# Optimization experiments

Hardware: AMD Instinct MI355X
Metric: run time of the kernel (lower is better)

Reference implementation:

```python
import jax, jax.numpy as jnp
import numpy as np

B = 8
D_MODEL = 512
N_HEADS = 8
D_HEAD = 64
D_FF = 2048
N_ENC = 4
N_DEC = 4
SRC_LEN = 512
TGT_LEN = 512
PRED_LEN = 96
SRC_SIZE = 16
TGT_SIZE = 8
EPS = 1e-5
W_SCALE = 0.02


def setup_inputs() -> dict:
    key = jax.random.key(0)
    ks = iter(jax.random.split(key, 64))

    def w(shape):
        return jax.random.normal(next(ks), shape, dtype=jnp.float32) * W_SCALE

    d, f = D_MODEL, D_FF
    inp = {
        "src": jax.random.normal(next(ks), (B, SRC_LEN, SRC_SIZE), dtype=jnp.float32),
        "tgt": jax.random.normal(next(ks), (B, TGT_LEN, TGT_SIZE), dtype=jnp.float32),
        "src_pos_emb": w((SRC_LEN, d)),
        "tgt_pos_emb": w((TGT_LEN, d)),
        "src_lin_w": w((SRC_SIZE, d)), "src_lin_b": jnp.zeros((d,), jnp.float32),
        "tgt_lin_w": w((TGT_SIZE, d)), "tgt_lin_b": jnp.zeros((d,), jnp.float32),
        # encoder stacks [N_ENC, ...]
        "enc_wq": w((N_ENC, d, d)), "enc_wk": w((N_ENC, d, d)),
        "enc_wv": w((N_ENC, d, d)), "enc_wo": w((N_ENC, d, d)),
        "enc_ff1_w": w((N_ENC, d, f)), "enc_ff1_b": jnp.zeros((N_ENC, f), jnp.float32),
        "enc_ff2_w": w((N_ENC, f, d)), "enc_ff2_b": jnp.zeros((N_ENC, d), jnp.float32),
        "enc_ln1_g": jnp.ones((N_ENC, d), jnp.float32), "enc_ln1_b": jnp.zeros((N_ENC, d), jnp.float32),
        "enc_ln2_g": jnp.ones((N_ENC, d), jnp.float32), "enc_ln2_b": jnp.zeros((N_ENC, d), jnp.float32),
        # decoder stacks [N_DEC, ...]
        "dec_sa_wq": w((N_DEC, d, d)), "dec_sa_wk": w((N_DEC, d, d)),
        "dec_sa_wv": w((N_DEC, d, d)), "dec_sa_wo": w((N_DEC, d, d)),
        "dec_ca_wq": w((N_DEC, d, d)), "dec_ca_wk": w((N_DEC, d, d)),
        "dec_ca_wv": w((N_DEC, d, d)), "dec_ca_wo": w((N_DEC, d, d)),
        "dec_ff1_w": w((N_DEC, d, f)), "dec_ff1_b": jnp.zeros((N_DEC, f), jnp.float32),
        "dec_ff2_w": w((N_DEC, f, d)), "dec_ff2_b": jnp.zeros((N_DEC, d), jnp.float32),
        "dec_ln1_g": jnp.ones((N_DEC, d), jnp.float32), "dec_ln1_b": jnp.zeros((N_DEC, d), jnp.float32),
        "dec_ln2_g": jnp.ones((N_DEC, d), jnp.float32), "dec_ln2_b": jnp.zeros((N_DEC, d), jnp.float32),
        "dec_ln3_g": jnp.ones((N_DEC, d), jnp.float32), "dec_ln3_b": jnp.zeros((N_DEC, d), jnp.float32),
        "proj_w": w((d, TGT_SIZE)), "proj_b": jnp.zeros((TGT_SIZE,), jnp.float32),
    }
    return inp


def layer_norm(x, g, b):
    mu = jnp.mean(x, axis=-1, keepdims=True)
    var = jnp.mean(jnp.square(x - mu), axis=-1, keepdims=True)
    return (x - mu) * jax.lax.rsqrt(var + EPS) * g + b


def mha(x_q, x_kv, wq, wk, wv, wo, mask):
    Bq, Lq, _ = x_q.shape
    Lk = x_kv.shape[1]
    q = (x_q @ wq).reshape(Bq, Lq, N_HEADS, D_HEAD)
    k = (x_kv @ wk).reshape(Bq, Lk, N_HEADS, D_HEAD)
    v = (x_kv @ wv).reshape(Bq, Lk, N_HEADS, D_HEAD)
    scores = jnp.einsum("bqhd,bkhd->bhqk", q, k) / jnp.sqrt(
        jnp.asarray(D_HEAD, jnp.float32))
    if mask is not None:
        scores = scores + mask  # broadcast over batch/heads
    attn = jax.nn.softmax(scores, axis=-1)
    ctx = jnp.einsum("bhqk,bkhd->bqhd", attn, v).reshape(Bq, Lq, N_HEADS * D_HEAD)
    return ctx @ wo


def dec_self_mask():
    # get_subsequence_mask with pt=0: -inf on last PRED_LEN key columns
    m = jnp.zeros((TGT_LEN, TGT_LEN), jnp.float32)
    return m.at[:, -PRED_LEN:].set(-jnp.inf)


def reference(src, tgt, src_pos_emb, tgt_pos_emb, src_lin_w, src_lin_b,
              tgt_lin_w, tgt_lin_b,
              enc_wq, enc_wk, enc_wv, enc_wo, enc_ff1_w, enc_ff1_b,
              enc_ff2_w, enc_ff2_b, enc_ln1_g, enc_ln1_b, enc_ln2_g, enc_ln2_b,
              dec_sa_wq, dec_sa_wk, dec_sa_wv, dec_sa_wo,
              dec_ca_wq, dec_ca_wk, dec_ca_wv, dec_ca_wo,
              dec_ff1_w, dec_ff1_b, dec_ff2_w, dec_ff2_b,
              dec_ln1_g, dec_ln1_b, dec_ln2_g, dec_ln2_b, dec_ln3_g, dec_ln3_b,
              proj_w, proj_b):
    # input projections + positional embedding (dropout disabled, eval mode)
    enc_x = src_pos_emb[None] + src @ src_lin_w + src_lin_b
    dec_x = tgt_pos_emb[None] + tgt @ tgt_lin_w + tgt_lin_b

    # encoder (enc_self_attn_mask is None)
    for i in range(N_ENC):
        a = mha(enc_x, enc_x, enc_wq[i], enc_wk[i], enc_wv[i], enc_wo[i], None)
        enc_x = layer_norm(a + enc_x, enc_ln1_g[i], enc_ln1_b[i])
        h = jax.nn.relu(enc_x @ enc_ff1_w[i] + enc_ff1_b[i]) @ enc_ff2_w[i] + enc_ff2_b[i]
        enc_x = layer_norm(h + enc_x, enc_ln2_g[i], enc_ln2_b[i])

    sa_mask = dec_self_mask()  # [tgt_len, tgt_len]
    for i in range(N_DEC):
        a = mha(dec_x, dec_x, dec_sa_wq[i], dec_sa_wk[i], dec_sa_wv[i],
                dec_sa_wo[i], sa_mask)
        dec_x = layer_norm(a + dec_x, dec_ln1_g[i], dec_ln1_b[i])
        a = mha(dec_x, enc_x, dec_ca_wq[i], dec_ca_wk[i], dec_ca_wv[i],
                dec_ca_wo[i], None)
        dec_x = layer_norm(a + dec_x, dec_ln2_g[i], dec_ln2_b[i])
        h = jax.nn.relu(dec_x @ dec_ff1_w[i] + dec_ff1_b[i]) @ dec_ff2_w[i] + dec_ff2_b[i]
        dec_x = layer_norm(h + dec_x, dec_ln3_g[i], dec_ln3_b[i])

    return dec_x @ proj_w + proj_b  # [B, tgt_len, tgt_size]
```

## Files before the change

### kernel.cpp

```cpp
#include <hip/hip_runtime.h>
#include <hip/hip_bf16.h>
#include <math.h>

#define D_MODEL 512
#define N_HEADS 8
#define D_HEAD  64
#define D_FF    2048
#define SEQ     512
#define BATCH   8
#define ROWS    (BATCH * SEQ)
#define PRED_LEN 96
#define KLEN_MASKED (SEQ - PRED_LEN)
#define LN_EPS  1e-5f

typedef float  f32x4 __attribute__((ext_vector_type(4)));
typedef short  s16x8 __attribute__((ext_vector_type(8)));

__device__ __forceinline__ float bf2f(ushort u) {
    union { unsigned int i; float f; } c; c.i = ((unsigned int)u) << 16; return c.f;
}
__device__ __forceinline__ ushort f2bf(float v) {
    __hip_bfloat16 h = __float2bfloat16(v);
    return *(ushort*)&h;
}
__device__ __forceinline__ void gl_lds16(const void* g, void* lds) {
    __builtin_amdgcn_global_load_lds(
        (const __attribute__((address_space(1))) unsigned int*)g,
        (__attribute__((address_space(3))) unsigned int*)lds, 16, 0, 0);
}

struct GDesc {
    const ushort* A; int lda;
    const ushort* Bt; int ldb;
    ushort* C; int ldc;
    int N; int K;
    const float* bias; int relu;
    ushort* VT; int vcol0;
};

template<int BN>
__device__ __forceinline__ void gemm_body(const GDesc& d)
{
    constexpr int NW = BN / 32;
    __shared__ __attribute__((aligned(16))) ushort As[2][128 * 32];
    __shared__ __attribute__((aligned(16))) ushort Bs[2][BN * 32];
    const int tid = threadIdx.x;
    const int w = tid >> 6, lane = tid & 63;
    const int l16 = lane & 15, quad = lane >> 4;
    const int m0 = blockIdx.y * 128, n0 = blockIdx.x * BN;
    const ushort* Ab = d.A + (size_t)m0 * d.lda;
    const ushort* Bb = d.Bt + (size_t)n0 * d.ldb;
    const int wm = (w >> 1) * 64, wn = (w & 1) * (BN / 2);
    const int nk = d.K >> 5;

    auto stage = [&](int buf, int k0) {
        #pragma unroll
        for (int q = 0; q < 2; ++q) {
            int c = (q * 4 + w) * 64 + lane;
            int row = c >> 2, ch = (c & 3) ^ ((row >> 1) & 3);
            gl_lds16(Ab + (size_t)row * d.lda + k0 + ch * 8,
                     (void*)(As[buf] + (size_t)(q * 4 + w) * 512));
        }
        #pragma unroll
        for (int q = 0; q < BN / 64; ++q) {
            int c = (q * 4 + w) * 64 + lane;
            int row = c >> 2, ch = (c & 3) ^ ((row >> 1) & 3);
            gl_lds16(Bb + (size_t)row * d.ldb + k0 + ch * 8,
                     (void*)(Bs[buf] + (size_t)(q * 4 + w) * 512));
        }
    };

    f32x4 acc[4][NW];
    #pragma unroll
    for (int i = 0; i < 4; ++i)
        #pragma unroll
        for (int j = 0; j < NW; ++j) acc[i][j] = (f32x4)0.f;

    auto compute = [&](int buf) {
        s16x8 af[4];
        #pragma unroll
        for (int i = 0; i < 4; ++i) {
            int r = wm + i * 16 + l16;
            af[i] = *(const s16x8*)(As[buf] + (size_t)r * 32 + (quad ^ ((r >> 1) & 3)) * 8);
        }
        #pragma unroll
        for (int j = 0; j < NW; ++j) {
            int r = wn + j * 16 + l16;
            s16x8 bfr = *(const s16x8*)(Bs[buf] + (size_t)r * 32 + (quad ^ ((r >> 1) & 3)) * 8);
            #pragma unroll
            for (int i = 0; i < 4; ++i)
                acc[i][j] = __builtin_amdgcn_mfma_f32_16x16x32_bf16(af[i], bfr, acc[i][j], 0, 0, 0);
        }
    };

    stage(0, 0);
    __syncthreads();
    int cur = 0;
    for (int t = 0; t < nk - 1; ++t) {
        stage(cur ^ 1, (t + 1) << 5);
        compute(cur);
        __syncthreads();
        cur ^= 1;
    }
    compute(cur);

    const bool isv = (d.VT != nullptr) && (n0 >= d.vcol0);
    if (isv) {
        #pragma unroll
        for (int i = 0; i < 4; ++i) {
            int mrow = m0 + wm + i * 16 + quad * 4;
            int b = mrow >> 9, pbase = mrow & 511;
            #pragma unroll
            for (int j = 0; j < NW; ++j) {
                int cv = n0 + wn + j * 16 + l16 - d.vcol0;
                int h = cv >> 6, dd = cv & 63;
                union { ushort u[4]; uint2 v; } pk;
                #pragma unroll
                for (int r = 0; r < 4; ++r) pk.u[r] = f2bf(acc[i][j][r]);
                *(uint2*)(d.VT + ((size_t)((b * 8 + h) * 64 + dd) * 512 + pbase)) = pk.v;
            }
        }
    } else {
        #pragma unroll
        for (int i = 0; i < 4; ++i) {
            #pragma unroll
            for (int j = 0; j < NW; ++j) {
                int col = n0 + wn + j * 16 + l16;
                float bv = d.bias ? d.bias[col] : 0.f;
                #pragma unroll
                for (int r = 0; r < 4; ++r) {
                    float v = acc[i][j][r] + bv;
                    if (d.relu) v = fmaxf(v, 0.f);
                    d.C[(size_t)(m0 + wm + i * 16 + quad * 4 + r) * d.ldc + col] = f2bf(v);
                }
            }
        }
    }
}

template<int BN>
__global__ __launch_bounds__(256) void gemm_one(GDesc d)
{
    if ((int)(blockIdx.x * BN) < d.N) gemm_body<BN>(d);
}

__global__ __launch_bounds__(256) void gemm_two(GDesc d0, GDesc d1)
{
    const GDesc& d = blockIdx.z ? d1 : d0;
    if ((int)(blockIdx.x * 64) < d.N) gemm_body<64>(d);
}

struct SKDesc {
    const ushort* A; int lda;
    const ushort* Bt; int ldb;
    float* P;
    int K;
};

__global__ __launch_bounds__(256) void gemm_sk(SKDesc d)
{
    __shared__ __attribute__((aligned(16))) ushort As[2][128 * 32];
    __shared__ __attribute__((aligned(16))) ushort Bs[2][64 * 32];
    const int tid = threadIdx.x;
    const int w = tid >> 6, lane = tid & 63;
    const int l16 = lane & 15, quad = lane >> 4;
    const int m0 = blockIdx.y * 128, n0 = blockIdx.x * 64;
    const int slice = blockIdx.z;
    const int kb = slice * (d.K >> 1);
    const int nk = d.K >> 6;
    const ushort* Ab = d.A + (size_t)m0 * d.lda + kb;
    const ushort* Bb = d.Bt + (size_t)n0 * d.ldb + kb;
    const int wm = (w >> 1) * 64, wn = (w & 1) * 32;

    auto stage = [&](int buf, int k0) {
        #pragma unroll
        for (int q = 0; q < 2; ++q) {
            int c = (q * 4 + w) * 64 + lane;
            int row = c >> 2, ch = (c & 3) ^ ((row >> 1) & 3);
            gl_lds16(Ab + (size_t)row * d.lda + k0 + ch * 8,
                     (void*)(As[buf] + (size_t)(q * 4 + w) * 512));
        }
        {
            int c = w * 64 + lane;
            int row = c >> 2, ch = (c & 3) ^ ((row >> 1) & 3);
            gl_lds16(Bb + (size_t)row * d.ldb + k0 + ch * 8,
                     (void*)(Bs[buf] + (size_t)w * 512));
        }
    };

    f32x4 acc[4][2];
    #pragma unroll
    for (int i = 0; i < 4; ++i)
        #pragma unroll
        for (int j = 0; j < 2; ++j) acc[i][j] = (f32x4)0.f;

    auto compute = [&](int buf) {
        s16x8 af[4];
        #pragma unroll
        for (int i = 0; i < 4; ++i) {
            int r = wm + i * 16 + l16;
            af[i] = *(const s16x8*)(As[buf] + (size_t)r * 32 + (quad ^ ((r >> 1) & 3)) * 8);
        }
        #pragma unroll
        for (int j = 0; j < 2; ++j) {
            int r = wn + j * 16 + l16;
            s16x8 bfr = *(const s16x8*)(Bs[buf] + (size_t)r * 32 + (quad ^ ((r >> 1) & 3)) * 8);
            #pragma unroll
            for (int i = 0; i < 4; ++i)
                acc[i][j] = __builtin_amdgcn_mfma_f32_16x16x32_bf16(af[i], bfr, acc[i][j], 0, 0, 0);
        }
    };

    stage(0, 0);
    __syncthreads();
    int cur = 0;
    for (int t = 0; t < nk - 1; ++t) {
        stage(cur ^ 1, (t + 1) << 5);
        compute(cur);
        __syncthreads();
        cur ^= 1;
    }
    compute(cur);

    float* P = d.P + (size_t)slice * ((size_t)ROWS * 512);
    #pragma unroll
    for (int i = 0; i < 4; ++i) {
        #pragma unroll
        for (int j = 0; j < 2; ++j) {
            int col = n0 + wn + j * 16 + l16;
            #pragma unroll
            for (int r = 0; r < 4; ++r)
                P[(size_t)(m0 + wm + i * 16 + quad * 4 + r) * 512 + col] = acc[i][j][r];
        }
    }
}

__global__ __launch_bounds__(256) void flash_attn(
    const ushort* __restrict__ Q, int ldq,
    const ushort* __restrict__ K, int ldk,
    const ushort* __restrict__ Vt,
    ushort* __restrict__ O, int ldo, int klen)
{
    __shared__ __attribute__((aligned(16))) ushort KVs[8192];
    __shared__ __attribute__((aligned(16))) ushort Es[4][2048];
    const int tid = threadIdx.x, w = tid >> 6, lane = tid & 63;
    const int l16 = lane & 15, quad = lane >> 4;
    const int bh = blockIdx.y, b = bh >> 3, h = bh & 7;
    const int q0 = blockIdx.x * 64;

    const ushort* Qb = Q + (size_t)(b * SEQ) * ldq + h * D_HEAD;
    const ushort* Kb = K + (size_t)(b * SEQ) * ldk + h * D_HEAD;

    s16x8 af0, af1;
    {
        const ushort* qr = Qb + (size_t)(q0 + w * 16 + l16) * ldq + quad * 8;
        af0 = *(const s16x8*)(qr);
        af1 = *(const s16x8*)(qr + 32);
    }

    f32x4 sc[32];

    #pragma unroll
    for (int kc = 0; kc < 4; ++kc) {
        #pragma unroll
        for (int it = 0; it < 4; ++it) {
            int cc = (it * 4 + w) * 64 + lane;
            int row = cc >> 3;
            int dch = (cc & 7) ^ (row & 7);
            gl_lds16(Kb + (size_t)(kc * 128 + row) * ldk + dch * 8,
                     (void*)(KVs + (size_t)(it * 4 + w) * 512));
        }
        __syncthreads();
        #pragma unroll
        for (int kt = 0; kt < 8; ++kt) {
            int r0 = kt * 16 + l16;
            s16x8 b0 = *(const s16x8*)(KVs + r0 * 64 + ((quad)     ^ (r0 & 7)) * 8);
            s16x8 b1 = *(const s16x8*)(KVs + r0 * 64 + ((4 + quad) ^ (r0 & 7)) * 8);
            f32x4 a = __builtin_amdgcn_mfma_f32_16x16x32_bf16(af0, b0, (f32x4)0.f, 0, 0, 0);
            sc[kc * 8 + kt] = __builtin_amdgcn_mfma_f32_16x16x32_bf16(af1, b1, a, 0, 0, 0);
        }
        __syncthreads();
    }

    float inv[4];
    #pragma unroll
    for (int r = 0; r < 4; ++r) {
        float m = -1e30f;
        #pragma unroll
        for (int j = 0; j < 32; ++j) {
            bool valid = (j * 16 + l16) < klen;
            m = valid ? fmaxf(m, sc[j][r]) : m;
        }
        m = fmaxf(m, __shfl_xor(m, 1));
        m = fmaxf(m, __shfl_xor(m, 2));
        m = fmaxf(m, __shfl_xor(m, 4));
        m = fmaxf(m, __shfl_xor(m, 8));
        float ssum = 0.f;
        #pragma unroll
        for (int j = 0; j < 32; ++j) {
            bool valid = (j * 16 + l16) < klen;
            float e = valid ? __expf((sc[j][r] - m) * 0.125f) : 0.f;
            sc[j][r] = e;
            ssum += e;
        }
        ssum += __shfl_xor(ssum, 1);
        ssum += __shfl_xor(ssum, 2);
        ssum += __shfl_xor(ssum, 4);
        ssum += __shfl_xor(ssum, 8);
        inv[r] = 1.f / ssum;
    }

    f32x4 oacc[4];
    #pragma unroll
    for (int jd = 0; jd < 4; ++jd) oacc[jd] = (f32x4)0.f;
    const ushort* Vb = Vt + (size_t)bh * (D_HEAD * SEQ);
    #pragma unroll
    for (int kc = 0; kc < 4; ++kc) {
        #pragma unroll
        for (int it = 0; it < 4; ++it) {
            int cc = (it * 4 + w) * 64 + lane;
            int d = cc >> 4;
            int kch = (cc & 15) ^ (d & 15);
            gl_lds16(Vb + (size_t)d * SEQ + kc * 128 + kch * 8,
                     (void*)(KVs + (size_t)(it * 4 + w) * 512));
        }
        #pragma unroll
        for (int j = 0; j < 8; ++j) {
            int lcj = j * 2 + (l16 >> 3);
            #pragma unroll
            for (int r = 0; r < 4; ++r) {
                int m = quad * 4 + r;
                Es[w][m * 128 + (lcj ^ m) * 8 + (l16 & 7)] = f2bf(sc[kc * 8 + j][r]);
            }
        }
        __syncthreads();
        #pragma unroll
        for (int ks = 0; ks < 4; ++ks) {
            int lc = ks * 4 + quad;
            s16x8 ea = *(const s16x8*)(&Es[w][l16 * 128 + (lc ^ l16) * 8]);
            #pragma unroll
            for (int jd = 0; jd < 4; ++jd) {
                int row = jd * 16 + l16;
                s16x8 vb = *(const s16x8*)(KVs + row * 128 + (lc ^ l16) * 8);
                oacc[jd] = __builtin_amdgcn_mfma_f32_16x16x32_bf16(ea, vb, oacc[jd], 0, 0, 0);
            }
        }
        __syncthreads();
    }

    ushort* Ob = O + (size_t)(b * SEQ) * ldo + h * D_HEAD;
    #pragma unroll
    for (int jd = 0; jd < 4; ++jd)
        #pragma unroll
        for (int r = 0; r < 4; ++r)
            Ob[(size_t)(q0 + w * 16 + quad * 4 + r) * ldo + jd * 16 + l16] =
                f2bf(oacc[jd][r] * inv[r]);
}

struct AttnPtrs { const float* p[48]; };
struct FfPtrs   { const float* p[16]; };

__global__ __launch_bounds__(256) void repack_attn(AttnPtrs L, ushort* __restrict__ out)
{
    int z = blockIdx.z;
    const float* in = L.p[z];
    ushort* o = out + (size_t)z * 262144;
    __shared__ float t[32][33];
    int n0 = blockIdx.x * 32, k0 = blockIdx.y * 32;
    int tx = threadIdx.x & 31, ty = threadIdx.x >> 5;
    #pragma unroll
    for (int r = 0; r < 4; ++r)
        t[ty + r * 8][tx] = in[(size_t)(k0 + ty + r * 8) * 512 + n0 + tx];
    __syncthreads();
    #pragma unroll
    for (int r = 0; r < 4; ++r)
        o[(size_t)(n0 + ty + r * 8) * 512 + k0 + tx] = f2bf(t[tx][ty + r * 8]);
}

__global__ __launch_bounds__(256) void repack_ff(FfPtrs L, ushort* __restrict__ out)
{
    int z = blockIdx.y;
    int Kd = (z < 8) ? 512 : 2048, Nd = (z < 8) ? 2048 : 512;
    const float* in = L.p[z];
    ushort* o = out + (size_t)z * (512 * 2048);
    int t = blockIdx.x;
    int tn = Nd / 32;
    int n0 = (t % tn) * 32, k0 = (t / tn) * 32;
    __shared__ float ts[32][33];
    int tx = threadIdx.x & 31, ty = threadIdx.x >> 5;
    #pragma unroll
    for (int r = 0; r < 4; ++r)
        ts[ty + r * 8][tx] = in[(size_t)(k0 + ty + r * 8) * Nd + n0 + tx];
    __syncthreads();
    #pragma unroll
    for (int r = 0; r < 4; ++r)
        o[(size_t)(n0 + ty + r * 8) * Kd + k0 + tx] = f2bf(ts[tx][ty + r * 8]);
}

__global__ __launch_bounds__(256) void input_proj2(
    const float* __restrict__ x0, const float* __restrict__ w0,
    const float* __restrict__ b0, const float* __restrict__ p0,
    float* __restrict__ o0_32, ushort* __restrict__ o0_b, int in0,
    const float* __restrict__ x1, const float* __restrict__ w1,
    const float* __restrict__ b1, const float* __restrict__ p1,
    float* __restrict__ o1_32, ushort* __restrict__ o1_b, int in1)
{
    const int z = blockIdx.y;
    const float* x = z ? x1 : x0;  const float* w = z ? w1 : w0;
    const float* bias = z ? b1 : b0; const float* pos = z ? p1 : p0;
    float* out32 = z ? o1_32 : o0_32; ushort* outb = z ? o1_b : o0_b;
    int in_size = z ? in1 : in0;
    int idx = blockIdx.x * 256 + threadIdx.x;
    int col = idx & (D_MODEL - 1);
    int row = idx >> 9;
    int l   = row & (SEQ - 1);
    const float* xr = x + (size_t)row * in_size;
    float acc = bias[col] + pos[(size_t)l * D_MODEL + col];
    for (int t = 0; t < in_size; ++t) acc += xr[t] * w[(size_t)t * D_MODEL + col];
    out32[idx] = acc;
    outb[idx]  = f2bf(acc);
}

__global__ __launch_bounds__(256) void add_ln2(
    const float* __restrict__ p, const float* __restrict__ gb,
    const float* __restrict__ x,
    const float* __restrict__ g, const float* __restrict__ b,
    float* __restrict__ out32, ushort* __restrict__ outb)
{
    const int row  = blockIdx.x * 4 + (threadIdx.x >> 6);
    const int lane = threadIdx.x & 63;
    const int c0   = lane * 8;
    const size_t base = (size_t)row * D_MODEL + c0;
    const float* p1 = p + (size_t)ROWS * 512;
    f32x4 a0 = *(const f32x4*)(p + base),  a1 = *(const f32x4*)(p + base + 4);
    f32x4 c0v= *(const f32x4*)(p1 + base), c1v= *(const f32x4*)(p1 + base + 4);
    f32x4 x0 = *(const f32x4*)(x + base),  x1 = *(const f32x4*)(x + base + 4);
    float v[8];
    #pragma unroll
    for (int j = 0; j < 4; ++j) {
        v[j]     = a0[j] + c0v[j] + x0[j];
        v[4 + j] = a1[j] + c1v[j] + x1[j];
    }
    if (gb) {
        f32x4 gb0 = *(const f32x4*)(gb + c0), gb1 = *(const f32x4*)(gb + c0 + 4);
        #pragma unroll
        for (int j = 0; j < 4; ++j) { v[j] += gb0[j]; v[4 + j] += gb1[j]; }
    }
    float s = 0.f;
    #pragma unroll
    for (int j = 0; j < 8; ++j) s += v[j];
    #pragma unroll
    for (int off = 32; off; off >>= 1) s += __shfl_xor(s, off);
    float mu = s * (1.f / D_MODEL);
    float q = 0.f;
    #pragma unroll
    for (int j = 0; j < 8; ++j) { v[j] -= mu; q += v[j] * v[j]; }
    #pragma unroll
    for (int off = 32; off; off >>= 1) q += __shfl_xor(q, off);
    float rs = rsqrtf(q * (1.f / D_MODEL) + LN_EPS);
    f32x4 g0 = *(const f32x4*)(g + c0), g1 = *(const f32x4*)(g + c0 + 4);
    f32x4 b0 = *(const f32x4*)(b + c0), b1 = *(const f32x4*)(b + c0 + 4);
    f32x4 y0, y1;
    union { ushort u[8]; s16x8 w; } pk;
    #pragma unroll
    for (int j = 0; j < 4; ++j) {
        y0[j] = v[j]     * rs * g0[j] + b0[j];
        y1[j] = v[4 + j] * rs * g1[j] + b1[j];
        pk.u[j]     = f2bf(y0[j]);
        pk.u[4 + j] = f2bf(y1[j]);
    }
    *(f32x4*)(out32 + base)     = y0;
    *(f32x4*)(out32 + base + 4) = y1;
    *(s16x8*)(outb + base)      = pk.w;
}

__global__ __launch_bounds__(256) void final_proj(
    const float* __restrict__ X, const float* __restrict__ W,
    const float* __restrict__ b, float* __restrict__ out)
{
    const int row  = blockIdx.x * 4 + (threadIdx.x >> 6);
    const int lane = threadIdx.x & 63;
    const float* xr = X + (size_t)row * D_MODEL + lane * 8;
    f32x4 x0 = *(const f32x4*)(xr), x1 = *(const f32x4*)(xr + 4);
    const float* wr = W + (size_t)lane * 64;
    f32x4 pa = (f32x4)0.f, pb = (f32x4)0.f;
    #pragma unroll
    for (int j = 0; j < 8; ++j) {
        float xv = (j < 4) ? x0[j] : x1[j - 4];
        f32x4 w0 = *(const f32x4*)(wr + j * 8);
        f32x4 w1 = *(const f32x4*)(wr + j * 8 + 4);
        #pragma unroll
        for (int c = 0; c < 4; ++c) { pa[c] += xv * w0[c]; pb[c] += xv * w1[c]; }
    }
    #pragma unroll
    for (int off = 32; off; off >>= 1) {
        #pragma unroll
        for (int c = 0; c < 4; ++c) {
            pa[c] += __shfl_xor(pa[c], off);
            pb[c] += __shfl_xor(pb[c], off);
        }
    }
    if (lane == 0) {
        float* o = out + (size_t)row * 8;
        #pragma unroll
        for (int c = 0; c < 4; ++c) { o[c] = pa[c] + b[c]; o[4 + c] = pb[c] + b[4 + c]; }
    }
}

extern "C" void kernel_launch(void* const* d_in, const int* in_sizes, int n_in,
                              void* d_out, int out_size, void* d_ws, size_t ws_size,
                              hipStream_t stream)
{
    const float* src         = (const float*)d_in[0];
    const float* tgt         = (const float*)d_in[1];
    const float* src_pos     = (const float*)d_in[2];
    const float* tgt_pos     = (const float*)d_in[3];
    const float* src_lin_w   = (const float*)d_in[4];
    const float* src_lin_b   = (const float*)d_in[5];
    const float* tgt_lin_w   = (const float*)d_in[6];
    const float* tgt_lin_b   = (const float*)d_in[7];
    const float* enc_wq      = (const float*)d_in[8];
    const float* enc_wk      = (const float*)d_in[9];
    const float* enc_wv      = (const float*)d_in[10];
    const float* enc_wo      = (const float*)d_in[11];
    const float* enc_ff1_w   = (const float*)d_in[12];
    const float* enc_ff1_b   = (const float*)d_in[13];
    const float* enc_ff2_w   = (const float*)d_in[14];
    const float* enc_ff2_b   = (const float*)d_in[15];
    const float* enc_ln1_g   = (const float*)d_in[16];
    const float* enc_ln1_b   = (const float*)d_in[17];
    const float* enc_ln2_g   = (const float*)d_in[18];
    const float* enc_ln2_b   = (const float*)d_in[19];
    const float* dec_sa_wq   = (const float*)d_in[20];
    const float* dec_sa_wk   = (const float*)d_in[21];
    const float* dec_sa_wv   = (const float*)d_in[22];
    const float* dec_sa_wo   = (const float*)d_in[23];
    const float* dec_ca_wq   = (const float*)d_in[24];
    const float* dec_ca_wk   = (const float*)d_in[25];
    const float* dec_ca_wv   = (const float*)d_in[26];
    const float* dec_ca_wo   = (const float*)d_in[27];
    const float* dec_ff1_w   = (const float*)d_in[28];
    const float* dec_ff1_b   = (const float*)d_in[29];
    const float* dec_ff2_w   = (const float*)d_in[30];
    const float* dec_ff2_b   = (const float*)d_in[31];
    const float* dec_ln1_g   = (const float*)d_in[32];
    const float* dec_ln1_b   = (const float*)d_in[33];
    const float* dec_ln2_g   = (const float*)d_in[34];
    const float* dec_ln2_b   = (const float*)d_in[35];
    const float* dec_ln3_g   = (const float*)d_in[36];
    const float* dec_ln3_b   = (const float*)d_in[37];
    const float* proj_w      = (const float*)d_in[38];
    const float* proj_b      = (const float*)d_in[39];

    char* p = (char*)d_ws;
    auto carve = [&](size_t bytes) { char* r = p; p += (bytes + 255) & ~(size_t)255; return r; };
    ushort* enc_xb = (ushort*)carve((size_t)ROWS * D_MODEL * 2);
    ushort* dec_xb = (ushort*)carve((size_t)ROWS * D_MODEL * 2);
    float*  enc_x32= (float*) carve((size_t)ROWS * D_MODEL * 4);
    float*  dec_x32= (float*) carve((size_t)ROWS * D_MODEL * 4);
    ushort* qkvb   = (ushort*)carve((size_t)ROWS * 1536 * 2);
    ushort* qb     = (ushort*)carve((size_t)ROWS * D_MODEL * 2);
    ushort* kvb    = (ushort*)carve((size_t)ROWS * 1024 * 2);
    ushort* ctxb   = (ushort*)carve((size_t)ROWS * D_MODEL * 2);
    float*  pf     = (float*) carve((size_t)2 * ROWS * D_MODEL * 4);
    ushort* ffhb   = (ushort*)carve((size_t)ROWS * D_FF * 2);
    ushort* vt     = (ushort*)carve((size_t)64 * D_HEAD * SEQ * 2);
    ushort* wa     = (ushort*)carve((size_t)48 * 262144 * 2);
    ushort* wf     = (ushort*)carve((size_t)16 * 1048576 * 2);

    const dim3 blk(256);

    {
        AttnPtrs A;
        for (int i = 0; i < 4; ++i) {
            const size_t o = (size_t)i * 262144;
            A.p[i * 3 + 0] = enc_wq + o;  A.p[i * 3 + 1] = enc_wk + o;  A.p[i * 3 + 2] = enc_wv + o;
            A.p[12 + i] = enc_wo + o;
            A.p[16 + i * 3 + 0] = dec_sa_wq + o; A.p[16 + i * 3 + 1] = dec_sa_wk + o;
            A.p[16 + i * 3 + 2] = dec_sa_wv + o;
            A.p[28 + i] = dec_sa_wo + o;
            A.p[32 + i * 2 + 0] = dec_ca_wk + o; A.p[32 + i * 2 + 1] = dec_ca_wv + o;
            A.p[40 + i] = dec_ca_wq + o;
            A.p[44 + i] = dec_ca_wo + o;
        }
        repack_attn<<<dim3(16, 16, 48), blk, 0, stream>>>(A, wa);
        FfPtrs F;
        for (int i = 0; i < 4; ++i) {
            F.p[0 + i]  = enc_ff1_w + (size_t)i * 1048576;
            F.p[4 + i]  = dec_ff1_w + (size_t)i * 1048576;
            F.p[8 + i]  = enc_ff2_w + (size_t)i * 1048576;
            F.p[12 + i] = dec_ff2_w + (size_t)i * 1048576;
        }
        repack_ff<<<dim3(1024, 16), blk, 0, stream>>>(F, wf);
    }

    auto mkd = [&](const ushort* A, int lda, const ushort* Bt, int ldb,
                   ushort* C, int ldc, int N, int K,
                   const float* bias, int relu, ushort* VT, int vcol0) {
        GDesc d; d.A = A; d.lda = lda; d.Bt = Bt; d.ldb = ldb;
        d.C = C; d.ldc = ldc; d.N = N; d.K = K;
        d.bias = bias; d.relu = relu; d.VT = VT; d.vcol0 = vcol0;
        return d;
    };
    auto g64 = [&](const GDesc& d) {
        gemm_one<64><<<dim3(d.N / 64, ROWS / 128), blk, 0, stream>>>(d);
    };
    auto gsk = [&](const ushort* A, int lda, const ushort* Bt, int K) {
        SKDesc d; d.A = A; d.lda = lda; d.Bt = Bt; d.ldb = K; d.P = pf; d.K = K;
        gemm_sk<<<dim3(8, ROWS / 128, 2), blk, 0, stream>>>(d);
    };

    input_proj2<<<dim3(ROWS * D_MODEL / 256, 2), blk, 0, stream>>>(
        src, src_lin_w, src_lin_b, src_pos, enc_x32, enc_xb, 16,
        tgt, tgt_lin_w, tgt_lin_b, tgt_pos, dec_x32, dec_xb, 8);

    for (int i = 0; i < 4; ++i) {
        g64(mkd(enc_xb, 512, wa + (size_t)(i * 3) * 262144, 512, qkvb, 1536,
                1536, 512, nullptr, 0, vt, 1024));
        flash_attn<<<dim3(8, 64), blk, 0, stream>>>(qkvb, 1536, qkvb + 512, 1536, vt,
                                                    ctxb, D_MODEL, SEQ);
        gsk(ctxb, 512, wa + (size_t)(12 + i) * 262144, 512);
        add_ln2<<<ROWS / 4, blk, 0, stream>>>(pf, nullptr, enc_x32,
                                              enc_ln1_g + i * 512, enc_ln1_b + i * 512,
                                              enc_x32, enc_xb);
        g64(mkd(enc_xb, 512, wf + (size_t)i * 1048576, 512, ffhb, 2048,
                2048, 512, enc_ff1_b + i * 2048, 1, nullptr, 0));
        gsk(ffhb, 2048, wf + (size_t)(8 + i) * 1048576, 2048);
        add_ln2<<<ROWS / 4, blk, 0, stream>>>(pf, enc_ff2_b + i * 512, enc_x32,
                                              enc_ln2_g + i * 512, enc_ln2_b + i * 512,
                                              enc_x32, enc_xb);
    }

    for (int i = 0; i < 4; ++i) {
        g64(mkd(dec_xb, 512, wa + (size_t)(16 + i * 3) * 262144, 512, qkvb, 1536,
                1536, 512, nullptr, 0, vt, 1024));
        flash_attn<<<dim3(8, 64), blk, 0, stream>>>(qkvb, 1536, qkvb + 512, 1536, vt,
                                                    ctxb, D_MODEL, KLEN_MASKED);
        gsk(ctxb, 512, wa + (size_t)(28 + i) * 262144, 512);
        add_ln2<<<ROWS / 4, blk, 0, stream>>>(pf, nullptr, dec_x32,
                                              dec_ln1_g + i * 512, dec_ln1_b + i * 512,
                                              dec_x32, dec_xb);
        {
            GDesc dq = mkd(dec_xb, 512, wa + (size_t)(40 + i) * 262144, 512, qb, 512,
                           512, 512, nullptr, 0, nullptr, 0);
            GDesc dkv = mkd(enc_xb, 512, wa + (size_t)(32 + i * 2) * 262144, 512, kvb, 1024,
                            1024, 512, nullptr, 0, vt, 512);
            gemm_two<<<dim3(16, ROWS / 128, 2), blk, 0, stream>>>(dq, dkv);
        }
        flash_attn<<<dim3(8, 64), blk, 0, stream>>>(qb, 512, kvb, 1024, vt,
                                                    ctxb, D_MODEL, SEQ);
        gsk(ctxb, 512, wa + (size_t)(44 + i) * 262144, 512);
        add_ln2<<<ROWS / 4, blk, 0, stream>>>(pf, nullptr, dec_x32,
                                              dec_ln2_g + i * 512, dec_ln2_b + i * 512,
                                              dec_x32, dec_xb);
        g64(mkd(dec_xb, 512, wf + (size_t)(4 + i) * 1048576, 512, ffhb, 2048,
                2048, 512, dec_ff1_b + i * 2048, 1, nullptr, 0));
        gsk(ffhb, 2048, wf + (size_t)(12 + i) * 1048576, 2048);
        add_ln2<<<ROWS / 4, blk, 0, stream>>>(pf, dec_ff2_b + i * 512, dec_x32,
                                              dec_ln3_g + i * 512, dec_ln3_b + i * 512,
                                              dec_x32, dec_xb);
    }

    final_proj<<<ROWS / 4, blk, 0, stream>>>(dec_x32, proj_w, proj_b, (float*)d_out);
}
```

Before: 1.386 ms.

## Replace LDS-staged GEMM tiles with direct global-to-register double-buffered loads

The GEMM and split-K kernels no longer stage A/B tiles through shared memory with global_load_lds and block barriers. Each lane now loads its MFMA fragments straight from global memory into registers, using a two-deep register ping-pong, and the K loop length becomes a compile-time template parameter so it unrolls fully. This removes LDS traffic and __syncthreads, but gives up cross-wave reuse of the loaded tiles, so global/L2 traffic per block rises and register pressure goes up. Correctness depends on every launch site matching the hardcoded NK (all GEMMs with K=512 or K=2048).

```diff
diff --git a/kernel.cpp b/kernel.cpp
--- a/kernel.cpp
+++ b/kernel.cpp
@@ -38,37 +38,24 @@
     ushort* VT; int vcol0;
 };
 
-template<int BN>
-__device__ __forceinline__ void gemm_body(const GDesc& d)
+template<int BN, int NK>
+__device__ __forceinline__ void gemm_reg(const GDesc& d)
 {
     constexpr int NW = BN / 32;
-    __shared__ __attribute__((aligned(16))) ushort As[2][128 * 32];
-    __shared__ __attribute__((aligned(16))) ushort Bs[2][BN * 32];
     const int tid = threadIdx.x;
     const int w = tid >> 6, lane = tid & 63;
     const int l16 = lane & 15, quad = lane >> 4;
     const int m0 = blockIdx.y * 128, n0 = blockIdx.x * BN;
-    const ushort* Ab = d.A + (size_t)m0 * d.lda;
-    const ushort* Bb = d.Bt + (size_t)n0 * d.ldb;
     const int wm = (w >> 1) * 64, wn = (w & 1) * (BN / 2);
-    const int nk = d.K >> 5;
-
-    auto stage = [&](int buf, int k0) {
-        #pragma unroll
-        for (int q = 0; q < 2; ++q) {
-            int c = (q * 4 + w) * 64 + lane;
-            int row = c >> 2, ch = (c & 3) ^ ((row >> 1) & 3);
-            gl_lds16(Ab + (size_t)row * d.lda + k0 + ch * 8,
-                     (void*)(As[buf] + (size_t)(q * 4 + w) * 512));
-        }
-        #pragma unroll
-        for (int q = 0; q < BN / 64; ++q) {
-            int c = (q * 4 + w) * 64 + lane;
-            int row = c >> 2, ch = (c & 3) ^ ((row >> 1) & 3);
-            gl_lds16(Bb + (size_t)row * d.ldb + k0 + ch * 8,
-                     (void*)(Bs[buf] + (size_t)(q * 4 + w) * 512));
-        }
-    };
+
+    const ushort* Ab[4];
+    #pragma unroll
+    for (int i = 0; i < 4; ++i)
+        Ab[i] = d.A + (size_t)(m0 + wm + i * 16 + l16) * d.lda + quad * 8;
+    const ushort* Bb[NW];
+    #pragma unroll
+    for (int j = 0; j < NW; ++j)
+        Bb[j] = d.Bt + (size_t)(n0 + wn + j * 16 + l16) * d.ldb + quad * 8;
 
     f32x4 acc[4][NW];
     #pragma unroll
@@ -76,33 +63,40 @@
         #pragma unroll
         for (int j = 0; j < NW; ++j) acc[i][j] = (f32x4)0.f;
 
-    auto compute = [&](int buf) {
-        s16x8 af[4];
-        #pragma unroll
-        for (int i = 0; i < 4; ++i) {
-            int r = wm + i * 16 + l16;
-            af[i] = *(const s16x8*)(As[buf] + (size_t)r * 32 + (quad ^ ((r >> 1) & 3)) * 8);
-        }
-        #pragma unroll
-        for (int j = 0; j < NW; ++j) {
-            int r = wn + j * 16 + l16;
-            s16x8 bfr = *(const s16x8*)(Bs[buf] + (size_t)r * 32 + (quad ^ ((r >> 1) & 3)) * 8);
+    s16x8 aP[4], aQ[4];
+    s16x8 bP[NW], bQ[NW];
+    #pragma unroll
+    for (int i = 0; i < 4; ++i) aP[i] = *(const s16x8*)(Ab[i]);
+    #pragma unroll
+    for (int j = 0; j < NW; ++j) bP[j] = *(const s16x8*)(Bb[j]);
+
+    #pragma unroll
+    for (int t = 0; t < NK; t += 2) {
+        if (t + 1 < NK) {
+            #pragma unroll
+            for (int i = 0; i < 4; ++i) aQ[i] = *(const s16x8*)(Ab[i] + (t + 1) * 32);
+            #pragma unroll
+            for (int j = 0; j < NW; ++j) bQ[j] = *(const s16x8*)(Bb[j] + (t + 1) * 32);
+        }
+        #pragma unroll
+        for (int j = 0; j < NW; ++j)
             #pragma unroll
             for (int i = 0; i < 4; ++i)
-                acc[i][j] = __builtin_amdgcn_mfma_f32_16x16x32_bf16(af[i], bfr, acc[i][j], 0, 0, 0);
-        }
-    };
-
-    stage(0, 0);
-    __syncthreads();
-    int cur = 0;
-    for (int t = 0; t < nk - 1; ++t) {
-        stage(cur ^ 1, (t + 1) << 5);
-        compute(cur);
-        __syncthreads();
-        cur ^= 1;
-    }
-    compute(cur);
+                acc[i][j] = __builtin_amdgcn_mfma_f32_16x16x32_bf16(aP[i], bP[j], acc[i][j], 0, 0, 0);
+        if (t + 2 < NK) {
+            #pragma unroll
+            for (int i = 0; i < 4; ++i) aP[i] = *(const s16x8*)(Ab[i] + (t + 2) * 32);
+            #pragma unroll
+            for (int j = 0; j < NW; ++j) bP[j] = *(const s16x8*)(Bb[j] + (t + 2) * 32);
+        }
+        if (t + 1 < NK) {
+            #pragma unroll
+            for (int j = 0; j < NW; ++j)
+                #pragma unroll
+                for (int i = 0; i < 4; ++i)
+                    acc[i][j] = __builtin_amdgcn_mfma_f32_16x16x32_bf16(aQ[i], bQ[j], acc[i][j], 0, 0, 0);
+        }
+    }
 
     const bool isv = (d.VT != nullptr) && (n0 >= d.vcol0);
     if (isv) {
@@ -138,16 +132,16 @@
     }
 }
 
-template<int BN>
+template<int BN, int NK>
 __global__ __launch_bounds__(256) void gemm_one(GDesc d)
 {
-    if ((int)(blockIdx.x * BN) < d.N) gemm_body<BN>(d);
+    if ((int)(blockIdx.x * BN) < d.N) gemm_reg<BN, NK>(d);
 }
 
 __global__ __launch_bounds__(256) void gemm_two(GDesc d0, GDesc d1)
 {
     const GDesc& d = blockIdx.z ? d1 : d0;
-    if ((int)(blockIdx.x * 64) < d.N) gemm_body<64>(d);
+    if ((int)(blockIdx.x * 64) < d.N) gemm_reg<64, 16>(d);
 }
 
 struct SKDesc {
@@ -157,36 +151,25 @@
     int K;
 };
 
+template<int NK>
 __global__ __launch_bounds__(256) void gemm_sk(SKDesc d)
 {
-    __shared__ __attribute__((aligned(16))) ushort As[2][128 * 32];
-    __shared__ __attribute__((aligned(16))) ushort Bs[2][64 * 32];
     const int tid = threadIdx.x;
     const int w = tid >> 6, lane = tid & 63;
     const int l16 = lane & 15, quad = lane >> 4;
     const int m0 = blockIdx.y * 128, n0 = blockIdx.x * 64;
     const int slice = blockIdx.z;
     const int kb = slice * (d.K >> 1);
-    const int nk = d.K >> 6;
-    const ushort* Ab = d.A + (size_t)m0 * d.lda + kb;
-    const ushort* Bb = d.Bt + (size_t)n0 * d.ldb + kb;
     const int wm = (w >> 1) * 64, wn = (w & 1) * 32;
 
-    auto stage = [&](int buf, int k0) {
-        #pragma unroll
-        for (int q = 0; q < 2; ++q) {
-            int c = (q * 4 + w) * 64 + lane;
-            int row = c >> 2, ch = (c & 3) ^ ((row >> 1) & 3);
-            gl_lds16(Ab + (size_t)row * d.lda + k0 + ch * 8,
-                     (void*)(As[buf] + (size_t)(q * 4 + w) * 512));
-        }
-        {
-            int c = w * 64 + lane;
-            int row = c >> 2, ch = (c & 3) ^ ((row >> 1) & 3);
-            gl_lds16(Bb + (size_t)row * d.ldb + k0 + ch * 8,
-                     (void*)(Bs[buf] + (size_t)w * 512));
-        }
-    };
+    const ushort* Ab[4];
+    #pragma unroll
+    for (int i = 0; i < 4; ++i)
+        Ab[i] = d.A + (size_t)(m0 + wm + i * 16 + l16) * d.lda + kb + quad * 8;
+    const ushort* Bb[2];
+    #pragma unroll
+    for (int j = 0; j < 2; ++j)
+        Bb[j] = d.Bt + (size_t)(n0 + wn + j * 16 + l16) * d.ldb + kb + quad * 8;
 
     f32x4 acc[4][2];
     #pragma unroll
@@ -194,33 +177,39 @@
         #pragma unroll
         for (int j = 0; j < 2; ++j) acc[i][j] = (f32x4)0.f;
 
-    auto compute = [&](int buf) {
-        s16x8 af[4];
-        #pragma unroll
-        for (int i = 0; i < 4; ++i) {
-            int r = wm + i * 16 + l16;
-            af[i] = *(const s16x8*)(As[buf] + (size_t)r * 32 + (quad ^ ((r >> 1) & 3)) * 8);
-        }
-        #pragma unroll
-        for (int j = 0; j < 2; ++j) {
-            int r = wn + j * 16 + l16;
-            s16x8 bfr = *(const s16x8*)(Bs[buf] + (size_t)r * 32 + (quad ^ ((r >> 1) & 3)) * 8);
+    s16x8 aP[4], aQ[4], bP[2], bQ[2];
+    #pragma unroll
+    for (int i = 0; i < 4; ++i) aP[i] = *(const s16x8*)(Ab[i]);
+    #pragma unroll
+    for (int j = 0; j < 2; ++j) bP[j] = *(const s16x8*)(Bb[j]);
+
+    #pragma unroll
+    for (int t = 0; t < NK; t += 2) {
+        if (t + 1 < NK) {
+            #pragma unroll
+            for (int i = 0; i < 4; ++i) aQ[i] = *(const s16x8*)(Ab[i] + (t + 1) * 32);
+            #pragma unroll
+            for (int j = 0; j < 2; ++j) bQ[j] = *(const s16x8*)(Bb[j] + (t + 1) * 32);
+        }
+        #pragma unroll
+        for (int j = 0; j < 2; ++j)
             #pragma unroll
             for (int i = 0; i < 4; ++i)
-                acc[i][j] = __builtin_amdgcn_mfma_f32_16x16x32_bf16(af[i], bfr, acc[i][j], 0, 0, 0);
-        }
-    };
-
-    stage(0, 0);
-    __syncthreads();
-    int cur = 0;
-    for (int t = 0; t < nk - 1; ++t) {
-        stage(cur ^ 1, (t + 1) << 5);
-        compute(cur);
-        __syncthreads();
-        cur ^= 1;
-    }
-    compute(cur);
+                acc[i][j] = __builtin_amdgcn_mfma_f32_16x16x32_bf16(aP[i], bP[j], acc[i][j], 0, 0, 0);
+        if (t + 2 < NK) {
+            #pragma unroll
+            for (int i = 0; i < 4; ++i) aP[i] = *(const s16x8*)(Ab[i] + (t + 2) * 32);
+            #pragma unroll
+            for (int j = 0; j < 2; ++j) bP[j] = *(const s16x8*)(Bb[j] + (t + 2) * 32);
+        }
+        if (t + 1 < NK) {
+            #pragma unroll
+            for (int j = 0; j < 2; ++j)
+                #pragma unroll
+                for (int i = 0; i < 4; ++i)
+                    acc[i][j] = __builtin_amdgcn_mfma_f32_16x16x32_bf16(aQ[i], bQ[j], acc[i][j], 0, 0, 0);
+        }
+    }
 
     float* P = d.P + (size_t)slice * ((size_t)ROWS * 512);
     #pragma unroll
@@ -603,11 +592,14 @@
         return d;
     };
     auto g64 = [&](const GDesc& d) {
-        gemm_one<64><<<dim3(d.N / 64, ROWS / 128), blk, 0, stream>>>(d);
+        gemm_one<64, 16><<<dim3(d.N / 64, ROWS / 128), blk, 0, stream>>>(d);
     };
     auto gsk = [&](const ushort* A, int lda, const ushort* Bt, int K) {
         SKDesc d; d.A = A; d.lda = lda; d.Bt = Bt; d.ldb = K; d.P = pf; d.K = K;
-        gemm_sk<<<dim3(8, ROWS / 128, 2), blk, 0, stream>>>(d);
+        if (K == 512)
+            gemm_sk<8><<<dim3(8, ROWS / 128, 2), blk, 0, stream>>>(d);
+        else
+            gemm_sk<32><<<dim3(8, ROWS / 128, 2), blk, 0, stream>>>(d);
     };
 
     input_proj2<<<dim3(ROWS * D_MODEL / 256, 2), blk, 0, stream>>>(
```

After: 2.107 ms. 1.52x slower.
